# Optimization experiments

Hardware: AMD Instinct MI355X
Metric: run time of the kernel (lower is better)

The kernel has to match this reference:

```python
import jax, jax.numpy as jnp
import numpy as np

N_HEADS = 12
HIDDEN = 768  # NOTE: d_head == hidden_size in this module (unusual)

def setup_inputs() -> dict:
    key = jax.random.key(0)
    ks = jax.random.split(key, 4)
    b, s = 8, 512
    d3 = 3 * N_HEADS * HIDDEN
    return {
        "x": jax.random.normal(ks[0], (b, s, HIDDEN), dtype=jnp.float32),
        "mask": jnp.zeros((b, 1, 1, s), dtype=jnp.float32),
        "w_qkv": jax.random.normal(ks[1], (d3, HIDDEN), dtype=jnp.float32) * 0.02,
        "b_qkv": jnp.zeros((d3,), dtype=jnp.float32),
        "w_o": jax.random.normal(ks[2], (HIDDEN, N_HEADS * HIDDEN), dtype=jnp.float32) * 0.02,
        "b_o": jnp.zeros((HIDDEN,), dtype=jnp.float32),
    }

def reference(x, mask, w_qkv, b_qkv, w_o, b_o):
    b, s, _ = x.shape
    nh = N_HEADS * HIDDEN
    qkv = x @ w_qkv.T + b_qkv                      # (b, s, 3*n*h)
    q, k, v = jnp.split(qkv, 3, axis=-1)           # each (b, s, n*h)
    def heads(t):
        return t.reshape(b, s, N_HEADS, HIDDEN).transpose(0, 2, 1, 3)  # (b, n, s, h)
    q, k, v = heads(q), heads(k), heads(v)
    scale = 1.0 / np.sqrt(HIDDEN).astype(np.float32)
    scores = jnp.einsum('bnqh,bnkh->bnqk', q, k) * scale  # (b, n, s_q, s_k)
    scores = scores + mask                         # additive mask broadcast
    a = jax.nn.softmax(scores, axis=-1)
    av = jnp.einsum('bnqk,bnkh->bnqh', a, v)       # (b, n, s, h)
    h = av.transpose(0, 2, 1, 3).reshape(b, s, nh) # (b, s, n*h)
    return h @ w_o.T + b_o                         # (b, s, hidden)
```

## Files before the change

### kernel.cpp

```cpp
#include <hip/hip_runtime.h>
#include <hip/hip_bf16.h>
#include <stdint.h>

#define AS1 __attribute__((address_space(1)))
#define AS3 __attribute__((address_space(3)))

typedef __attribute__((ext_vector_type(8))) __bf16 bf16x8;
typedef __attribute__((ext_vector_type(4))) float f32x4;
typedef unsigned short u16;
typedef __attribute__((ext_vector_type(8))) unsigned short u16x8;

#define B_    8
#define S_    512
#define NH_   12
#define HD_   768
#define NHD_  (NH_*HD_)
#define D3_   (3*NHD_)
#define QK_SCALE 0.03608439182435161f

__device__ __forceinline__ u16 f2bf(float x) {
  union { float f; unsigned u; } a; a.f = x;
  unsigned r = a.u + 0x7fffu + ((a.u >> 16) & 1u);
  return (u16)(r >> 16);
}
__device__ __forceinline__ float bf2f(u16 x) {
  union { unsigned u; float f; } a; a.u = ((unsigned)x) << 16; return a.f;
}

__device__ __forceinline__ void gload16(const void* g, void* l) {
  __builtin_amdgcn_global_load_lds((const AS1 void*)g, (AS3 void*)l, 16, 0, 0);
}

struct GP {
  const u16* A;
  const u16* B;
  int K, lda, ldb;
  long sA, sB;
  void* o0; void* o1; void* o2;
  const float* bias;
};

template<int MODE>
__global__ __launch_bounds__(256)
void gemm_bt(GP p) {
  __shared__ __align__(16) char smem[32768];
  const int tid  = threadIdx.x;
  const int wave = tid >> 6, lane = tid & 63;
  const int wr = wave >> 1, wc = wave & 1;
  const int bm0 = blockIdx.y * 128;
  const int bn0 = blockIdx.x * 128;
  const int z   = blockIdx.z;

  const u16* A  = p.A + (long)z * p.sA;
  const u16* Bm = p.B + (long)z * p.sB;

  f32x4 acc[4][4];
  const f32x4 zero4 = {0.f, 0.f, 0.f, 0.f};
#pragma unroll
  for (int i = 0; i < 4; ++i)
#pragma unroll
    for (int j = 0; j < 4; ++j) acc[i][j] = zero4;

  const int scolsw = ((lane & 7) ^ (lane >> 3)) * 8;
  const u16* gA = A  + (size_t)(bm0 + wave*8 + (lane>>3)) * p.lda + scolsw;
  const u16* gB = Bm + (size_t)(bn0 + wave*8 + (lane>>3)) * p.ldb + scolsw;
  char* ldsA = smem;
  char* ldsB = smem + 16384;
  char* stA  = ldsA + wave*1024;
  char* stB  = ldsB + wave*1024;

  const int aRow = (wr*64 + (lane&15)) * 128;
  const int bRow = (wc*64 + (lane&15)) * 128;
  const int csw  = lane & 7;
  const int cOff0 = (((lane>>4)    ) ^ csw) << 4;
  const int cOff1 = ((4 + (lane>>4)) ^ csw) << 4;

  for (int k0 = 0; k0 < p.K; k0 += 64) {
#pragma unroll
    for (int i = 0; i < 4; ++i) {
      gload16(gA + (size_t)i*32*p.lda, stA + i*4096);
      gload16(gB + (size_t)i*32*p.ldb, stB + i*4096);
    }
    gA += 64; gB += 64;
    __syncthreads();
#pragma unroll
    for (int kk = 0; kk < 2; ++kk) {
      const int cOff = kk ? cOff1 : cOff0;
      bf16x8 av[4], bv[4];
#pragma unroll
      for (int i = 0; i < 4; ++i)
        av[i] = *(const bf16x8*)(ldsA + aRow + i*2048 + cOff);
#pragma unroll
      for (int j = 0; j < 4; ++j)
        bv[j] = *(const bf16x8*)(ldsB + bRow + j*2048 + cOff);
#pragma unroll
      for (int i = 0; i < 4; ++i)
#pragma unroll
        for (int j = 0; j < 4; ++j)
          acc[i][j] = __builtin_amdgcn_mfma_f32_16x16x32_bf16(av[i], bv[j], acc[i][j], 0, 0, 0);
    }
    __syncthreads();
  }

  const int r0 = bm0 + wr*64 + ((lane>>4) << 2);
  const int c0 = bn0 + wc*64 + (lane&15);
#pragma unroll
  for (int i = 0; i < 4; ++i) {
#pragma unroll
    for (int j = 0; j < 4; ++j) {
      const int col = c0 + j*16;
#pragma unroll
      for (int r = 0; r < 4; ++r) {
        const int row = r0 + i*16 + r;
        const float v = acc[i][j][r];
        if constexpr (MODE == 0) {
          const float vb = v + p.bias[col];
          const int which = col / NHD_;
          const int rem = col - which*NHD_;
          const int n = rem / HD_;
          const int h = rem - n*HD_;
          const int bb = row >> 9, s = row & 511;
          const long zz = (long)(bb*NH_ + n);
          if (which == 0)      ((u16*)p.o0)[zz*(long)(S_*HD_) + (long)s*HD_ + h] = f2bf(vb);
          else if (which == 1) ((u16*)p.o1)[zz*(long)(S_*HD_) + (long)s*HD_ + h] = f2bf(vb);
          else                 ((u16*)p.o2)[zz*(long)(S_*HD_) + (long)h*S_  + s] = f2bf(vb);
        } else if constexpr (MODE == 1) {
          ((u16*)p.o0)[(long)z*S_*S_ + (long)row*S_ + col] = f2bf(v * QK_SCALE);
        } else if constexpr (MODE == 2) {
          const int bb = z / NH_, n = z - bb*NH_;
          ((u16*)p.o0)[(long)(bb*S_ + row)*NHD_ + n*HD_ + col] = f2bf(v);
        } else {
          ((float*)p.o0)[((long)z * gridDim.y * 128 + row) * HD_ + col] = v;
        }
      }
    }
  }
}

__global__ __launch_bounds__(256)
void softmax_rows(const u16* __restrict__ S, u16* __restrict__ P,
                  const float* __restrict__ maskc) {
  const int wave = threadIdx.x >> 6, lane = threadIdx.x & 63;
  const int rid = blockIdx.x * 4 + wave;
  const int z = rid >> 9;
  const int b = z / NH_;
  const u16x8 sv = *(const u16x8*)(S + (size_t)rid * S_ + lane*8);
  const float* mrow = maskc + (size_t)b * S_;
  float vals[8];
  float m = -3.4e38f;
#pragma unroll
  for (int j = 0; j < 8; ++j) {
    vals[j] = bf2f(sv[j]) + mrow[lane*8 + j];
    m = fmaxf(m, vals[j]);
  }
#pragma unroll
  for (int o = 32; o > 0; o >>= 1) m = fmaxf(m, __shfl_xor(m, o));
  float sum = 0.f;
#pragma unroll
  for (int j = 0; j < 8; ++j) { vals[j] = __expf(vals[j] - m); sum += vals[j]; }
#pragma unroll
  for (int o = 32; o > 0; o >>= 1) sum += __shfl_xor(sum, o);
  const float inv = 1.0f / sum;
  u16x8 pv;
#pragma unroll
  for (int j = 0; j < 8; ++j) pv[j] = f2bf(vals[j] * inv);
  *(u16x8*)(P + (size_t)rid * S_ + lane*8) = pv;
}

__global__ __launch_bounds__(256)
void cvt_bf16(const float4* __restrict__ in, ushort4* __restrict__ out, int n4) {
  const int i = blockIdx.x * 256 + threadIdx.x;
  if (i >= n4) return;
  const float4 v = in[i];
  ushort4 o;
  o.x = f2bf(v.x); o.y = f2bf(v.y); o.z = f2bf(v.z); o.w = f2bf(v.w);
  out[i] = o;
}

__global__ __launch_bounds__(256)
void combine_out(const float4* __restrict__ part, const float* __restrict__ b,
                 float4* __restrict__ out, int n4) {
  const int i = blockIdx.x * 256 + threadIdx.x;
  if (i >= n4) return;
  const float4 a0 = part[i];
  const float4 a1 = part[i + (size_t)n4];
  const float4 a2 = part[i + (size_t)2*n4];
  const float4 a3 = part[i + (size_t)3*n4];
  const int c = (i * 4) % HD_;
  float4 o;
  o.x = a0.x + a1.x + a2.x + a3.x + b[c];
  o.y = a0.y + a1.y + a2.y + a3.y + b[c+1];
  o.z = a0.z + a1.z + a2.z + a3.z + b[c+2];
  o.w = a0.w + a1.w + a2.w + a3.w + b[c+3];
  out[i] = o;
}

extern "C" void kernel_launch(void* const* d_in, const int* in_sizes, int n_in,
                              void* d_out, int out_size, void* d_ws, size_t ws_size,
                              hipStream_t stream) {
  const float* x     = (const float*)d_in[0];
  const float* mask  = (const float*)d_in[1];
  const float* w_qkv = (const float*)d_in[2];
  const float* b_qkv = (const float*)d_in[3];
  const float* w_o   = (const float*)d_in[4];
  const float* b_o   = (const float*)d_in[5];
  float* out = (float*)d_out;

  int bc = 0;
  for (int c = 8; c >= 1; c >>= 1)
    if (56623104UL + (unsigned long)c*35389440UL <= ws_size) { bc = c; break; }
  if (bc == 0) return;

  char* ws = (char*)d_ws;
  u16* wqb = (u16*)(ws);
  u16* wob = (u16*)(ws + 42467328L);
  u16* xb  = (u16*)(ws + 56623104L);
  long off = 56623104L + (long)bc*786432L;
  u16* Q   = (u16*)(ws + off);  off += (long)bc*9437184L;
  u16* Kb  = (u16*)(ws + off);  off += (long)bc*9437184L;
  u16* Vt  = (u16*)(ws + off);  off += (long)bc*9437184L;
  u16* Sb  = (u16*)(ws + off);
  u16* Pb  = Kb;
  u16* H   = Q;
  float* Part = (float*)Sb;

  cvt_bf16<<<dim3(D3_*HD_/4/256), dim3(256), 0, stream>>>((const float4*)w_qkv, (ushort4*)wqb, D3_*HD_/4);
  cvt_bf16<<<dim3(HD_*NHD_/4/256), dim3(256), 0, stream>>>((const float4*)w_o, (ushort4*)wob, HD_*NHD_/4);

  const int nchunks = B_ / bc;
  const int rows_c = bc * S_;
  const int zc = bc * NH_;

  for (int c = 0; c < nchunks; ++c) {
    const long row0 = (long)c * rows_c;

    cvt_bf16<<<dim3(rows_c*HD_/4/256), dim3(256), 0, stream>>>(
        (const float4*)(x + row0*HD_), (ushort4*)xb, rows_c*HD_/4);

    GP p1; p1.A = xb; p1.B = wqb; p1.K = HD_; p1.lda = HD_; p1.ldb = HD_;
    p1.sA = 0; p1.sB = 0; p1.o0 = Q; p1.o1 = Kb; p1.o2 = Vt; p1.bias = b_qkv;
    gemm_bt<0><<<dim3(D3_/128, rows_c/128, 1), dim3(256), 0, stream>>>(p1);

    GP p2; p2.A = Q; p2.B = Kb; p2.K = HD_; p2.lda = HD_; p2.ldb = HD_;
    p2.sA = (long)S_*HD_; p2.sB = (long)S_*HD_;
    p2.o0 = Sb; p2.o1 = nullptr; p2.o2 = nullptr; p2.bias = nullptr;
    gemm_bt<1><<<dim3(S_/128, S_/128, zc), dim3(256), 0, stream>>>(p2);

    softmax_rows<<<dim3(zc*S_/4), dim3(256), 0, stream>>>(Sb, Pb, mask + (long)c*bc*S_);

    GP p3; p3.A = Pb; p3.B = Vt; p3.K = S_; p3.lda = S_; p3.ldb = S_;
    p3.sA = (long)S_*S_; p3.sB = (long)S_*HD_;
    p3.o0 = H; p3.o1 = nullptr; p3.o2 = nullptr; p3.bias = nullptr;
    gemm_bt<2><<<dim3(HD_/128, S_/128, zc), dim3(256), 0, stream>>>(p3);

    GP p4; p4.A = H; p4.B = wob; p4.K = NHD_/4; p4.lda = NHD_; p4.ldb = NHD_;
    p4.sA = NHD_/4; p4.sB = NHD_/4;
    p4.o0 = Part; p4.o1 = nullptr; p4.o2 = nullptr; p4.bias = nullptr;
    gemm_bt<3><<<dim3(HD_/128, rows_c/128, 4), dim3(256), 0, stream>>>(p4);

    combine_out<<<dim3(rows_c*HD_/4/256), dim3(256), 0, stream>>>(
        (const float4*)Part, b_o, (float4*)(out + row0*HD_), rows_c*HD_/4);
  }
}
```

Before: 617.2 us.

## Replace 128x128 GEMM with double-buffered 256x256 tile kernel and swizzled grid

Replaces the single-buffered 128x128-tile GEMM used by all four matmul stages with a 512-thread 256x256-tile kernel. The new kernel uses 128 KB of double-buffered LDS filled by direct global-to-LDS loads, interleaves prefetch of the next K tiles with MFMA phases, and raises MFMA priority with setprio. The QKV projection also uses a grouped tile-index swizzle for L2 locality. The aim is more data reuse per tile and hiding load latency, at the cost of heavy LDS use (one block per CU) and fewer blocks for the small per-head GEMMs.

```diff
diff --git a/kernel.cpp b/kernel.cpp
--- a/kernel.cpp
+++ b/kernel.cpp
@@ -31,106 +31,175 @@
   __builtin_amdgcn_global_load_lds((const AS1 void*)g, (AS3 void*)l, 16, 0, 0);
 }
 
-struct GP {
-  const u16* A;
-  const u16* B;
-  int K, lda, ldb;
+__device__ __forceinline__ void wg_bar() {
+  asm volatile("" ::: "memory");
+  __builtin_amdgcn_s_barrier();
+  asm volatile("" ::: "memory");
+}
+
+struct GP2 {
+  const u16 *A, *B;
+  int lda, ldb;
   long sA, sB;
-  void* o0; void* o1; void* o2;
+  void *o0, *o1, *o2;
   const float* bias;
+  int mtMask, mtShift;
 };
 
-template<int MODE>
-__global__ __launch_bounds__(256)
-void gemm_bt(GP p) {
-  __shared__ __align__(16) char smem[32768];
-  const int tid  = threadIdx.x;
-  const int wave = tid >> 6, lane = tid & 63;
-  const int wr = wave >> 1, wc = wave & 1;
-  const int bm0 = blockIdx.y * 128;
-  const int bn0 = blockIdx.x * 128;
-  const int z   = blockIdx.z;
-
-  const u16* A  = p.A + (long)z * p.sA;
-  const u16* Bm = p.B + (long)z * p.sB;
-
-  f32x4 acc[4][4];
+#define LOADA(DST, BUF, MIB)                                                   \
+  _Pragma("unroll") for (int mi = 0; mi < 4; ++mi) {                           \
+    DST[mi][0] = *(const bf16x8*)((BUF) + rowA + (MIB + mi) * 2048 + cs0);     \
+    DST[mi][1] = *(const bf16x8*)((BUF) + rowA + (MIB + mi) * 2048 + cs1);     \
+  }
+#define LOADB(DST, BUF, NIB)                                                   \
+  _Pragma("unroll") for (int ni = 0; ni < 2; ++ni) {                           \
+    DST[ni][0] = *(const bf16x8*)((BUF) + rowB + (NIB + ni) * 2048 + cs0);     \
+    DST[ni][1] = *(const bf16x8*)((BUF) + rowB + (NIB + ni) * 2048 + cs1);     \
+  }
+#define MFMAQ(MI0, NI0, AV, BV)                                                \
+  __builtin_amdgcn_s_setprio(1);                                               \
+  _Pragma("unroll") for (int mi = 0; mi < 4; ++mi)                             \
+    _Pragma("unroll") for (int ni = 0; ni < 2; ++ni)                           \
+      _Pragma("unroll") for (int kk = 0; kk < 2; ++kk)                         \
+        acc[MI0 + mi][NI0 + ni] = __builtin_amdgcn_mfma_f32_16x16x32_bf16(     \
+            AV[mi][kk], BV[ni][kk], acc[MI0 + mi][NI0 + ni], 0, 0, 0);         \
+  __builtin_amdgcn_s_setprio(0);
+
+template<int NKT, int MODE, int SWZ>
+__global__ __launch_bounds__(512, 2)
+void gemm256(GP2 p) {
+  __shared__ __align__(16) char smem[131072];
+  char* ldsA0 = smem;
+  char* ldsA1 = smem + 32768;
+  char* ldsB0 = smem + 65536;
+  char* ldsB1 = smem + 98304;
+  const int tid = threadIdx.x, wid = tid >> 6, lane = tid & 63;
+  const int wm = wid >> 2, wn = wid & 3;
+
+  int m_idx, n_idx, z;
+  if constexpr (SWZ) {
+    const int cpx = (int)gridDim.x >> 3;
+    const int bid = (int)blockIdx.x;
+    const int tile = (bid & 7) * cpx + (bid >> 3);
+    m_idx = tile & p.mtMask; n_idx = tile >> p.mtShift; z = 0;
+  } else {
+    m_idx = blockIdx.y; n_idx = blockIdx.x; z = blockIdx.z;
+  }
+  const long bm0 = (long)m_idx * 256, bn0 = (long)n_idx * 256;
+
+  const int scol = ((tid & 7) ^ ((tid >> 3) & 7)) * 8;
+  const u16* gA = p.A + (long)z * p.sA + (bm0 + (tid >> 3)) * (long)p.lda + scol;
+  const u16* gB = p.B + (long)z * p.sB + (bn0 + (tid >> 3)) * (long)p.ldb + scol;
+  const int dW = wid * 1024;
+
+  auto stageA = [&](int kt) {
+    char* d = ((kt & 1) ? ldsA1 : ldsA0) + dW;
+    const u16* s = gA + kt * 64;
+    gload16(s,                      d);
+    gload16(s + (size_t) 64 * p.lda, d + 8192);
+    gload16(s + (size_t)128 * p.lda, d + 16384);
+    gload16(s + (size_t)192 * p.lda, d + 24576);
+  };
+  auto stageB = [&](int kt) {
+    char* d = ((kt & 1) ? ldsB1 : ldsB0) + dW;
+    const u16* s = gB + kt * 64;
+    gload16(s,                      d);
+    gload16(s + (size_t) 64 * p.ldb, d + 8192);
+    gload16(s + (size_t)128 * p.ldb, d + 16384);
+    gload16(s + (size_t)192 * p.ldb, d + 24576);
+  };
+
+  f32x4 acc[8][4];
   const f32x4 zero4 = {0.f, 0.f, 0.f, 0.f};
 #pragma unroll
-  for (int i = 0; i < 4; ++i)
+  for (int i = 0; i < 8; ++i)
 #pragma unroll
     for (int j = 0; j < 4; ++j) acc[i][j] = zero4;
 
-  const int scolsw = ((lane & 7) ^ (lane >> 3)) * 8;
-  const u16* gA = A  + (size_t)(bm0 + wave*8 + (lane>>3)) * p.lda + scolsw;
-  const u16* gB = Bm + (size_t)(bn0 + wave*8 + (lane>>3)) * p.ldb + scolsw;
-  char* ldsA = smem;
-  char* ldsB = smem + 16384;
-  char* stA  = ldsA + wave*1024;
-  char* stB  = ldsB + wave*1024;
-
-  const int aRow = (wr*64 + (lane&15)) * 128;
-  const int bRow = (wc*64 + (lane&15)) * 128;
-  const int csw  = lane & 7;
-  const int cOff0 = (((lane>>4)    ) ^ csw) << 4;
-  const int cOff1 = ((4 + (lane>>4)) ^ csw) << 4;
-
-  for (int k0 = 0; k0 < p.K; k0 += 64) {
-#pragma unroll
-    for (int i = 0; i < 4; ++i) {
-      gload16(gA + (size_t)i*32*p.lda, stA + i*4096);
-      gload16(gB + (size_t)i*32*p.ldb, stB + i*4096);
-    }
-    gA += 64; gB += 64;
-    __syncthreads();
-#pragma unroll
-    for (int kk = 0; kk < 2; ++kk) {
-      const int cOff = kk ? cOff1 : cOff0;
-      bf16x8 av[4], bv[4];
-#pragma unroll
-      for (int i = 0; i < 4; ++i)
-        av[i] = *(const bf16x8*)(ldsA + aRow + i*2048 + cOff);
-#pragma unroll
-      for (int j = 0; j < 4; ++j)
-        bv[j] = *(const bf16x8*)(ldsB + bRow + j*2048 + cOff);
-#pragma unroll
-      for (int i = 0; i < 4; ++i)
-#pragma unroll
-        for (int j = 0; j < 4; ++j)
-          acc[i][j] = __builtin_amdgcn_mfma_f32_16x16x32_bf16(av[i], bv[j], acc[i][j], 0, 0, 0);
-    }
-    __syncthreads();
-  }
-
-  const int r0 = bm0 + wr*64 + ((lane>>4) << 2);
-  const int c0 = bn0 + wc*64 + (lane&15);
-#pragma unroll
-  for (int i = 0; i < 4; ++i) {
-#pragma unroll
-    for (int j = 0; j < 4; ++j) {
-      const int col = c0 + j*16;
-#pragma unroll
-      for (int r = 0; r < 4; ++r) {
-        const int row = r0 + i*16 + r;
-        const float v = acc[i][j][r];
-        if constexpr (MODE == 0) {
-          const float vb = v + p.bias[col];
-          const int which = col / NHD_;
-          const int rem = col - which*NHD_;
-          const int n = rem / HD_;
-          const int h = rem - n*HD_;
+  const int rowA = (wm * 128 + (lane & 15)) * 128;
+  const int rowB = (wn * 64  + (lane & 15)) * 128;
+  const int cs0 = (((lane >> 4)    ) ^ (lane & 7)) << 4;
+  const int cs1 = ((4 + (lane >> 4)) ^ (lane & 7)) << 4;
+
+  stageA(0); stageB(0);
+  stageB(1); stageA(1);
+  asm volatile("s_waitcnt vmcnt(8)" ::: "memory");
+  wg_bar();
+
+  bf16x8 aF[4][2], b01[2][2], b23[2][2];
+
+  for (int i = 0; i < NKT / 2; ++i) {
+    const bool st = (i + 1 < NKT / 2);
+    const int kt2 = 2 * i + 2, kt3 = 2 * i + 3;
+
+    LOADA(aF, ldsA0, 0); LOADB(b01, ldsB0, 0);
+    wg_bar(); MFMAQ(0, 0, aF, b01); wg_bar();
+    LOADB(b23, ldsB0, 2);
+    wg_bar(); MFMAQ(0, 2, aF, b23); wg_bar();
+    LOADA(aF, ldsA0, 4);
+    if (st) stageB(kt2);
+    wg_bar(); MFMAQ(4, 0, aF, b01); wg_bar();
+    if (st) stageA(kt2);
+    wg_bar(); MFMAQ(4, 2, aF, b23);
+    if (st) { asm volatile("s_waitcnt vmcnt(8)" ::: "memory"); }
+    else    { asm volatile("s_waitcnt vmcnt(0)" ::: "memory"); }
+    wg_bar();
+
+    LOADA(aF, ldsA1, 0); LOADB(b01, ldsB1, 0);
+    wg_bar(); MFMAQ(0, 0, aF, b01); wg_bar();
+    LOADB(b23, ldsB1, 2);
+    wg_bar(); MFMAQ(0, 2, aF, b23); wg_bar();
+    LOADA(aF, ldsA1, 4);
+    if (st) stageB(kt3);
+    wg_bar(); MFMAQ(4, 0, aF, b01); wg_bar();
+    if (st) stageA(kt3);
+    wg_bar(); MFMAQ(4, 2, aF, b23);
+    if (st) { asm volatile("s_waitcnt vmcnt(8)" ::: "memory"); }
+    wg_bar();
+  }
+
+  const int r0 = (int)bm0 + wm * 128 + ((lane >> 4) << 2);
+  const int c0 = (int)bn0 + wn * 64 + (lane & 15);
+#pragma unroll
+  for (int mi = 0; mi < 8; ++mi) {
+#pragma unroll
+    for (int ni = 0; ni < 4; ++ni) {
+      const int col = c0 + ni * 16;
+      if constexpr (MODE == 0) {
+        const int which = col / NHD_;
+        const int rem = col - which * NHD_;
+        const int n = rem / HD_;
+        const int h = rem - n * HD_;
+        const float bs = p.bias[col];
+#pragma unroll
+        for (int r = 0; r < 4; ++r) {
+          const int row = r0 + mi * 16 + r;
+          const float v = acc[mi][ni][r] + bs;
           const int bb = row >> 9, s = row & 511;
-          const long zz = (long)(bb*NH_ + n);
-          if (which == 0)      ((u16*)p.o0)[zz*(long)(S_*HD_) + (long)s*HD_ + h] = f2bf(vb);
-          else if (which == 1) ((u16*)p.o1)[zz*(long)(S_*HD_) + (long)s*HD_ + h] = f2bf(vb);
-          else                 ((u16*)p.o2)[zz*(long)(S_*HD_) + (long)h*S_  + s] = f2bf(vb);
-        } else if constexpr (MODE == 1) {
-          ((u16*)p.o0)[(long)z*S_*S_ + (long)row*S_ + col] = f2bf(v * QK_SCALE);
-        } else if constexpr (MODE == 2) {
-          const int bb = z / NH_, n = z - bb*NH_;
-          ((u16*)p.o0)[(long)(bb*S_ + row)*NHD_ + n*HD_ + col] = f2bf(v);
-        } else {
-          ((float*)p.o0)[((long)z * gridDim.y * 128 + row) * HD_ + col] = v;
+          const long zz = (long)(bb * NH_ + n);
+          if (which == 0)      ((u16*)p.o0)[zz * (long)(S_*HD_) + (long)s * HD_ + h] = f2bf(v);
+          else if (which == 1) ((u16*)p.o1)[zz * (long)(S_*HD_) + (long)s * HD_ + h] = f2bf(v);
+          else                 ((u16*)p.o2)[zz * (long)(S_*HD_) + (long)h * S_  + s] = f2bf(v);
+        }
+      } else if constexpr (MODE == 1) {
+#pragma unroll
+        for (int r = 0; r < 4; ++r) {
+          const int row = r0 + mi * 16 + r;
+          ((u16*)p.o0)[(long)z * S_ * S_ + (long)row * S_ + col] = f2bf(acc[mi][ni][r] * QK_SCALE);
+        }
+      } else if constexpr (MODE == 2) {
+        const int bb = z / NH_, n = z - bb * NH_;
+#pragma unroll
+        for (int r = 0; r < 4; ++r) {
+          const int row = r0 + mi * 16 + r;
+          ((u16*)p.o0)[(long)(bb * S_ + row) * NHD_ + n * HD_ + col] = f2bf(acc[mi][ni][r]);
+        }
+      } else {
+        const long rowsTot = (long)gridDim.y * 256;
+#pragma unroll
+        for (int r = 0; r < 4; ++r) {
+          const int row = r0 + mi * 16 + r;
+          ((float*)p.o0)[((long)z * rowsTot + row) * HD_ + col] = acc[mi][ni][r];
         }
       }
     }
@@ -230,6 +299,8 @@
   const int nchunks = B_ / bc;
   const int rows_c = bc * S_;
   const int zc = bc * NH_;
+  const int Mt2 = rows_c / 256;
+  const int mtShift = __builtin_ctz(Mt2);
 
   for (int c = 0; c < nchunks; ++c) {
     const long row0 = (long)c * rows_c;
@@ -237,26 +308,30 @@
     cvt_bf16<<<dim3(rows_c*HD_/4/256), dim3(256), 0, stream>>>(
         (const float4*)(x + row0*HD_), (ushort4*)xb, rows_c*HD_/4);
 
-    GP p1; p1.A = xb; p1.B = wqb; p1.K = HD_; p1.lda = HD_; p1.ldb = HD_;
+    GP2 p1; p1.A = xb; p1.B = wqb; p1.lda = HD_; p1.ldb = HD_;
     p1.sA = 0; p1.sB = 0; p1.o0 = Q; p1.o1 = Kb; p1.o2 = Vt; p1.bias = b_qkv;
-    gemm_bt<0><<<dim3(D3_/128, rows_c/128, 1), dim3(256), 0, stream>>>(p1);
-
-    GP p2; p2.A = Q; p2.B = Kb; p2.K = HD_; p2.lda = HD_; p2.ldb = HD_;
+    p1.mtMask = Mt2 - 1; p1.mtShift = mtShift;
+    gemm256<12, 0, 1><<<dim3((D3_/256) * Mt2), dim3(512), 0, stream>>>(p1);
+
+    GP2 p2; p2.A = Q; p2.B = Kb; p2.lda = HD_; p2.ldb = HD_;
     p2.sA = (long)S_*HD_; p2.sB = (long)S_*HD_;
     p2.o0 = Sb; p2.o1 = nullptr; p2.o2 = nullptr; p2.bias = nullptr;
-    gemm_bt<1><<<dim3(S_/128, S_/128, zc), dim3(256), 0, stream>>>(p2);
+    p2.mtMask = 0; p2.mtShift = 0;
+    gemm256<12, 1, 0><<<dim3(2, 2, zc), dim3(512), 0, stream>>>(p2);
 
     softmax_rows<<<dim3(zc*S_/4), dim3(256), 0, stream>>>(Sb, Pb, mask + (long)c*bc*S_);
 
-    GP p3; p3.A = Pb; p3.B = Vt; p3.K = S_; p3.lda = S_; p3.ldb = S_;
+    GP2 p3; p3.A = Pb; p3.B = Vt; p3.lda = S_; p3.ldb = S_;
     p3.sA = (long)S_*S_; p3.sB = (long)S_*HD_;
     p3.o0 = H; p3.o1 = nullptr; p3.o2 = nullptr; p3.bias = nullptr;
-    gemm_bt<2><<<dim3(HD_/128, S_/128, zc), dim3(256), 0, stream>>>(p3);
-
-    GP p4; p4.A = H; p4.B = wob; p4.K = NHD_/4; p4.lda = NHD_; p4.ldb = NHD_;
+    p3.mtMask = 0; p3.mtShift = 0;
+    gemm256<8, 2, 0><<<dim3(3, 2, zc), dim3(512), 0, stream>>>(p3);
+
+    GP2 p4; p4.A = H; p4.B = wob; p4.lda = NHD_; p4.ldb = NHD_;
     p4.sA = NHD_/4; p4.sB = NHD_/4;
     p4.o0 = Part; p4.o1 = nullptr; p4.o2 = nullptr; p4.bias = nullptr;
-    gemm_bt<3><<<dim3(HD_/128, rows_c/128, 4), dim3(256), 0, stream>>>(p4);
+    p4.mtMask = 0; p4.mtShift = 0;
+    gemm256<36, 3, 0><<<dim3(3, rows_c/256, 4), dim3(512), 0, stream>>>(p4);
 
     combine_out<<<dim3(rows_c*HD_/4/256), dim3(256), 0, stream>>>(
         (const float4*)Part, b_o, (float4*)(out + row0*HD_), rows_c*HD_/4);
```

Result: no change. 625.1 us (+1.3%).

## Store Q/K row-major in QKV GEMM and vectorize V-transpose epilogue

Applied to the files above, without the earlier changes.

The QKV projection epilogue now writes Q and K straight into a single row-major [rows, 2*NHD] buffer instead of scattering them into per-head layouts. Batched GEMMs address heads through separate batch and head strides. The V-transposed store is packed into ushort4 writes along the sequence dimension, and softmax now runs in place on the score buffer. The aim is to cut the per-element division and modulo index math and the scattered 2-byte stores in the epilogue. In exchange, the QK GEMM reads Q and K with a larger leading dimension, and the H buffer uses a stride of 2*NHD.

```diff
diff --git a/kernel.cpp b/kernel.cpp
--- a/kernel.cpp
+++ b/kernel.cpp
@@ -16,6 +16,7 @@
 #define HD_   768
 #define NHD_  (NH_*HD_)
 #define D3_   (3*NHD_)
+#define QKLD_ (2*NHD_)
 #define QK_SCALE 0.03608439182435161f
 
 __device__ __forceinline__ u16 f2bf(float x) {
@@ -35,8 +36,8 @@
   const u16* A;
   const u16* B;
   int K, lda, ldb;
-  long sA, sB;
-  void* o0; void* o1; void* o2;
+  long sAb, sAn, sBb, sBn;
+  void* o0; void* o2;
   const float* bias;
 };
 
@@ -50,9 +51,10 @@
   const int bm0 = blockIdx.y * 128;
   const int bn0 = blockIdx.x * 128;
   const int z   = blockIdx.z;
-
-  const u16* A  = p.A + (long)z * p.sA;
-  const u16* Bm = p.B + (long)z * p.sB;
+  const int zb  = z / NH_, zn = z - zb * NH_;
+
+  const u16* A  = p.A + zb * p.sAb + zn * p.sAn;
+  const u16* Bm = p.B + zb * p.sBb + zn * p.sBn;
 
   f32x4 acc[4][4];
   const f32x4 zero4 = {0.f, 0.f, 0.f, 0.f};
@@ -104,47 +106,73 @@
 
   const int r0 = bm0 + wr*64 + ((lane>>4) << 2);
   const int c0 = bn0 + wc*64 + (lane&15);
-#pragma unroll
-  for (int i = 0; i < 4; ++i) {
-#pragma unroll
-    for (int j = 0; j < 4; ++j) {
-      const int col = c0 + j*16;
-#pragma unroll
-      for (int r = 0; r < 4; ++r) {
-        const int row = r0 + i*16 + r;
-        const float v = acc[i][j][r];
-        if constexpr (MODE == 0) {
-          const float vb = v + p.bias[col];
-          const int which = col / NHD_;
-          const int rem = col - which*NHD_;
-          const int n = rem / HD_;
-          const int h = rem - n*HD_;
-          const int bb = row >> 9, s = row & 511;
-          const long zz = (long)(bb*NH_ + n);
-          if (which == 0)      ((u16*)p.o0)[zz*(long)(S_*HD_) + (long)s*HD_ + h] = f2bf(vb);
-          else if (which == 1) ((u16*)p.o1)[zz*(long)(S_*HD_) + (long)s*HD_ + h] = f2bf(vb);
-          else                 ((u16*)p.o2)[zz*(long)(S_*HD_) + (long)h*S_  + s] = f2bf(vb);
-        } else if constexpr (MODE == 1) {
-          ((u16*)p.o0)[(long)z*S_*S_ + (long)row*S_ + col] = f2bf(v * QK_SCALE);
-        } else if constexpr (MODE == 2) {
-          const int bb = z / NH_, n = z - bb*NH_;
-          ((u16*)p.o0)[(long)(bb*S_ + row)*NHD_ + n*HD_ + col] = f2bf(v);
-        } else {
-          ((float*)p.o0)[((long)z * gridDim.y * 128 + row) * HD_ + col] = v;
+
+  if constexpr (MODE == 0) {
+    if (bn0 < QKLD_) {
+#pragma unroll
+      for (int i = 0; i < 4; ++i) {
+        u16* rbase = (u16*)p.o0 + (long)(r0 + i*16) * QKLD_;
+#pragma unroll
+        for (int j = 0; j < 4; ++j) {
+          const int col = c0 + j*16;
+          const float bs = p.bias[col];
+#pragma unroll
+          for (int r = 0; r < 4; ++r)
+            rbase[(long)r * QKLD_ + col] = f2bf(acc[i][j][r] + bs);
         }
       }
-    }
-  }
-}
-
-__global__ __launch_bounds__(256)
-void softmax_rows(const u16* __restrict__ S, u16* __restrict__ P,
-                  const float* __restrict__ maskc) {
+    } else {
+#pragma unroll
+      for (int i = 0; i < 4; ++i) {
+        const int rowq = r0 + i*16;
+        const int s0 = rowq & 511;
+        const int bb = rowq >> 9;
+#pragma unroll
+        for (int j = 0; j < 4; ++j) {
+          const int col = c0 + j*16;
+          const int vcol = col - QKLD_;
+          const int n = vcol / HD_;
+          const int h = vcol - n*HD_;
+          const float bs = p.bias[col];
+          ushort4 pk;
+          pk.x = f2bf(acc[i][j][0] + bs);
+          pk.y = f2bf(acc[i][j][1] + bs);
+          pk.z = f2bf(acc[i][j][2] + bs);
+          pk.w = f2bf(acc[i][j][3] + bs);
+          *(ushort4*)((u16*)p.o2 + (long)(bb*NH_ + n)*(S_*HD_) + (long)h*S_ + s0) = pk;
+        }
+      }
+    }
+  } else {
+#pragma unroll
+    for (int i = 0; i < 4; ++i) {
+#pragma unroll
+      for (int j = 0; j < 4; ++j) {
+        const int col = c0 + j*16;
+#pragma unroll
+        for (int r = 0; r < 4; ++r) {
+          const int row = r0 + i*16 + r;
+          const float v = acc[i][j][r];
+          if constexpr (MODE == 1) {
+            ((u16*)p.o0)[(long)z*S_*S_ + (long)row*S_ + col] = f2bf(v * QK_SCALE);
+          } else if constexpr (MODE == 2) {
+            ((u16*)p.o0)[(long)(zb*S_ + row)*QKLD_ + zn*HD_ + col] = f2bf(v);
+          } else {
+            ((float*)p.o0)[((long)z * gridDim.y * 128 + row) * HD_ + col] = v;
+          }
+        }
+      }
+    }
+  }
+}
+
+__global__ __launch_bounds__(256)
+void softmax_rows(u16* __restrict__ SP, const float* __restrict__ maskc) {
   const int wave = threadIdx.x >> 6, lane = threadIdx.x & 63;
   const int rid = blockIdx.x * 4 + wave;
   const int z = rid >> 9;
   const int b = z / NH_;
-  const u16x8 sv = *(const u16x8*)(S + (size_t)rid * S_ + lane*8);
+  const u16x8 sv = *(const u16x8*)(SP + (size_t)rid * S_ + lane*8);
   const float* mrow = maskc + (size_t)b * S_;
   float vals[8];
   float m = -3.4e38f;
@@ -164,7 +192,7 @@
   u16x8 pv;
 #pragma unroll
   for (int j = 0; j < 8; ++j) pv[j] = f2bf(vals[j] * inv);
-  *(u16x8*)(P + (size_t)rid * S_ + lane*8) = pv;
+  *(u16x8*)(SP + (size_t)rid * S_ + lane*8) = pv;
 }
 
 __global__ __launch_bounds__(256)
@@ -216,13 +244,11 @@
   u16* wob = (u16*)(ws + 42467328L);
   u16* xb  = (u16*)(ws + 56623104L);
   long off = 56623104L + (long)bc*786432L;
-  u16* Q   = (u16*)(ws + off);  off += (long)bc*9437184L;
-  u16* Kb  = (u16*)(ws + off);  off += (long)bc*9437184L;
+  u16* QKn = (u16*)(ws + off);  off += (long)bc*18874368L;
   u16* Vt  = (u16*)(ws + off);  off += (long)bc*9437184L;
-  u16* Sb  = (u16*)(ws + off);
-  u16* Pb  = Kb;
-  u16* H   = Q;
-  float* Part = (float*)Sb;
+  u16* SP  = (u16*)(ws + off);
+  u16* H   = QKn;
+  float* Part = (float*)SP;
 
   cvt_bf16<<<dim3(D3_*HD_/4/256), dim3(256), 0, stream>>>((const float4*)w_qkv, (ushort4*)wqb, D3_*HD_/4);
   cvt_bf16<<<dim3(HD_*NHD_/4/256), dim3(256), 0, stream>>>((const float4*)w_o, (ushort4*)wob, HD_*NHD_/4);
@@ -238,24 +264,28 @@
         (const float4*)(x + row0*HD_), (ushort4*)xb, rows_c*HD_/4);
 
     GP p1; p1.A = xb; p1.B = wqb; p1.K = HD_; p1.lda = HD_; p1.ldb = HD_;
-    p1.sA = 0; p1.sB = 0; p1.o0 = Q; p1.o1 = Kb; p1.o2 = Vt; p1.bias = b_qkv;
+    p1.sAb = 0; p1.sAn = 0; p1.sBb = 0; p1.sBn = 0;
+    p1.o0 = QKn; p1.o2 = Vt; p1.bias = b_qkv;
     gemm_bt<0><<<dim3(D3_/128, rows_c/128, 1), dim3(256), 0, stream>>>(p1);
 
-    GP p2; p2.A = Q; p2.B = Kb; p2.K = HD_; p2.lda = HD_; p2.ldb = HD_;
-    p2.sA = (long)S_*HD_; p2.sB = (long)S_*HD_;
-    p2.o0 = Sb; p2.o1 = nullptr; p2.o2 = nullptr; p2.bias = nullptr;
+    GP p2; p2.A = QKn; p2.B = QKn + NHD_; p2.K = HD_; p2.lda = QKLD_; p2.ldb = QKLD_;
+    p2.sAb = (long)S_*QKLD_; p2.sAn = HD_;
+    p2.sBb = (long)S_*QKLD_; p2.sBn = HD_;
+    p2.o0 = SP; p2.o2 = nullptr; p2.bias = nullptr;
     gemm_bt<1><<<dim3(S_/128, S_/128, zc), dim3(256), 0, stream>>>(p2);
 
-    softmax_rows<<<dim3(zc*S_/4), dim3(256), 0, stream>>>(Sb, Pb, mask + (long)c*bc*S_);
-
-    GP p3; p3.A = Pb; p3.B = Vt; p3.K = S_; p3.lda = S_; p3.ldb = S_;
-    p3.sA = (long)S_*S_; p3.sB = (long)S_*HD_;
-    p3.o0 = H; p3.o1 = nullptr; p3.o2 = nullptr; p3.bias = nullptr;
+    softmax_rows<<<dim3(zc*S_/4), dim3(256), 0, stream>>>(SP, mask + (long)c*bc*S_);
+
+    GP p3; p3.A = SP; p3.B = Vt; p3.K = S_; p3.lda = S_; p3.ldb = S_;
+    p3.sAb = (long)NH_*S_*S_; p3.sAn = (long)S_*S_;
+    p3.sBb = (long)NH_*S_*HD_; p3.sBn = (long)S_*HD_;
+    p3.o0 = H; p3.o2 = nullptr; p3.bias = nullptr;
     gemm_bt<2><<<dim3(HD_/128, S_/128, zc), dim3(256), 0, stream>>>(p3);
 
-    GP p4; p4.A = H; p4.B = wob; p4.K = NHD_/4; p4.lda = NHD_; p4.ldb = NHD_;
-    p4.sA = NHD_/4; p4.sB = NHD_/4;
-    p4.o0 = Part; p4.o1 = nullptr; p4.o2 = nullptr; p4.bias = nullptr;
+    GP p4; p4.A = H; p4.B = wob; p4.K = NHD_/4; p4.lda = QKLD_; p4.ldb = NHD_;
+    p4.sAb = 0; p4.sAn = NHD_/4;
+    p4.sBb = 0; p4.sBn = NHD_/4;
+    p4.o0 = Part; p4.o2 = nullptr; p4.bias = nullptr;
     gemm_bt<3><<<dim3(HD_/128, rows_c/128, 4), dim3(256), 0, stream>>>(p4);
 
     combine_out<<<dim3(rows_c*HD_/4/256), dim3(256), 0, stream>>>(
```

Result: no change. 613.5 us (-0.6%).
